# Kernel tuning notes

Measured on AMD Instinct MI355X. Metric: run time of the kernel, lower is better.

## Reference

```python
import jax, jax.numpy as jnp
import numpy as np

TOPK, ALPHA, BETA, EPS = 13, 1.0, 6.0, 1e-9
IMG = 1024.0

def _box_min_max(b):
    # b: [..., 5] cxcywhr -> per-box axis-aligned extents of rotated corners
    cx, cy, w, h, r = (b[..., i] for i in range(5))
    cos_r, sin_r = jnp.cos(r), jnp.sin(r)
    dx = w / 2 * cos_r
    dy = h / 2 * sin_r
    xc = jnp.stack([cx - dx, cx + dx, cx + dx, cx - dx], -1)
    yc = jnp.stack([cy - dy, cy - dy, cy + dy, cy + dy], -1)
    xr = cx[..., None] + (xc - cx[..., None]) * cos_r[..., None] - (yc - cy[..., None]) * sin_r[..., None]
    yr = cy[..., None] + (xc - cx[..., None]) * sin_r[..., None] + (yc - cy[..., None]) * cos_r[..., None]
    return xr.min(-1), xr.max(-1), yr.min(-1), yr.max(-1)

def batch_cxcywhr_iou(box1, box2, eps=EPS):
    # box1 [B,M1,5], box2 [B,M2,5] -> [B,M1,M2]
    mnx1, mxx1, mny1, mxy1 = (t[:, :, None] for t in _box_min_max(box1))
    mnx2, mxx2, mny2, mxy2 = (t[:, None, :] for t in _box_min_max(box2))
    iw = jnp.clip(jnp.minimum(mxx1, mxx2) - jnp.maximum(mnx1, mnx2), 0.0)
    ih = jnp.clip(jnp.minimum(mxy1, mxy2) - jnp.maximum(mny1, mny2), 0.0)
    inter = iw * ih
    a1 = (box1[..., 2] * box1[..., 3])[:, :, None]
    a2 = (box2[..., 2] * box2[..., 3])[:, None, :]
    return jnp.clip(inter / (a1 + a2 - inter + eps), 0.0, 1.0)

def check_points_inside_rboxes(points, rboxes):
    # points [L,2], rboxes [B,n,5] -> float mask [B,n,L]
    px, py = points[:, 0], points[:, 1]
    cx, cy, w, h, r = (rboxes[..., i][..., None] for i in range(5))  # [B,n,1]
    dx, dy = px - cx, py - cy
    cos_r, sin_r = jnp.cos(r), jnp.sin(r)
    xl = dx * cos_r + dy * sin_r
    yl = -dx * sin_r + dy * cos_r
    return ((jnp.abs(xl) <= w / 2) & (jnp.abs(yl) <= h / 2)).astype(jnp.float32)

def gather_topk_anchors(metrics, topk, topk_mask):
    # metrics [B,n,L] -> float {0,1} mask [B,n,L]
    B, n, L = metrics.shape
    _, idxs = jax.lax.top_k(metrics, topk)  # [B,n,topk]
    bi = jnp.arange(B)[:, None, None]
    gi = jnp.arange(n)[None, :, None]
    is_in_topk = jnp.zeros((B, n, L), metrics.dtype).at[bi, gi, idxs].add(1.0)
    return is_in_topk * topk_mask

def compute_max_iou_anchor(ious):
    # ious [B,n,L] -> one-hot over n of argmax gt per anchor, [B,n,L]
    idx = jnp.argmax(ious, axis=1)  # [B,L]
    return jnp.transpose(jax.nn.one_hot(idx, ious.shape[1], dtype=ious.dtype), (0, 2, 1))

def _make_anchor_points():
    pts = []
    for s in (8, 16, 32):
        g = int(IMG) // s
        xs = (jnp.arange(g, dtype=jnp.float32) + 0.5) * s
        yy, xx = jnp.meshgrid(xs, xs, indexing='ij')
        pts.append(jnp.stack([xx.ravel(), yy.ravel()], -1))
    return jnp.concatenate(pts, 0)  # [21504, 2]

def _rand_rboxes(key, shape, wh_lo, wh_hi):
    k1, k2, k3 = jax.random.split(key, 3)
    cxy = jax.random.uniform(k1, shape[:-1] + (2,), minval=0.0, maxval=IMG)
    wh = jax.random.uniform(k2, shape[:-1] + (2,), minval=wh_lo, maxval=wh_hi)
    r = jax.random.uniform(k3, shape[:-1] + (1,), minval=-np.pi, maxval=np.pi)
    return jnp.concatenate([cxy, wh, r], -1).astype(jnp.float32)

def setup_inputs() -> dict:
    key = jax.random.key(0)
    ks = jax.random.split(key, 6)
    B, L, C, n = 8, 21504, 15, 60
    return {
        'pred_scores': jax.random.uniform(ks[0], (B, L, C), dtype=jnp.float32),
        'pred_rboxes': _rand_rboxes(ks[1], (B, L, 5), 4.0, 120.0),
        'anchor_points': _make_anchor_points(),
        'gt_labels': jax.random.randint(ks[2], (B, n, 1), 0, C).astype(jnp.int64),
        'gt_bboxes': _rand_rboxes(ks[3], (B, n, 5), 20.0, 300.0),
        'gt_poses': jnp.zeros((B, n, 1, 3), jnp.float32),
        'gt_crowd': jax.random.randint(ks[4], (B, n, 1), 0, 2).astype(jnp.int32),
        'pad_gt_mask': jnp.ones((B, n, 1), jnp.float32),
        'bg_index': 15,
    }

def reference(pred_scores, pred_rboxes, anchor_points, gt_labels, gt_bboxes, gt_poses, gt_crowd, pad_gt_mask, bg_index):
    B, L, C = pred_scores.shape
    n = gt_bboxes.shape[1]
    labels = gt_labels[..., 0]  # [B,n]

    ious = batch_cxcywhr_iou(gt_bboxes, pred_rboxes)  # [B,n,L]
    ps = jnp.transpose(pred_scores, (0, 2, 1))  # [B,C,L]
    bbox_cls_scores = jnp.take_along_axis(ps, jnp.broadcast_to(labels[:, :, None], (B, n, L)), axis=1)
    alignment_metrics = bbox_cls_scores ** ALPHA * ious ** BETA

    is_in_gts = check_points_inside_rboxes(anchor_points, gt_bboxes)
    is_in_topk = gather_topk_anchors(alignment_metrics * is_in_gts, TOPK, pad_gt_mask)
    mask_positive = is_in_topk * is_in_gts * pad_gt_mask
    mask_positive_sum = mask_positive.sum(axis=1)  # [B,L]

    # resolve anchors assigned to multiple gts by max IoU (identity when none)
    mask_multiple = jnp.broadcast_to((mask_positive_sum[:, None, :] > 1), (B, n, L))
    mask_positive = jnp.where(mask_multiple, compute_max_iou_anchor(ious), mask_positive)
    mask_positive_sum = mask_positive.sum(axis=1)

    assigned_gt_index = jnp.argmax(mask_positive, axis=1)  # [B,L]
    flat_idx = assigned_gt_index + jnp.arange(B)[:, None] * n

    assigned_labels = labels.reshape(-1)[flat_idx]
    assigned_labels = jnp.where(mask_positive_sum > 0, assigned_labels, bg_index)

    assigned_rboxes = gt_bboxes.reshape(-1, 5)[flat_idx.reshape(-1)].reshape(B, L, 5)

    assigned_scores = jax.nn.one_hot(assigned_labels, C + 1, dtype=pred_scores.dtype)
    keep = jnp.array([i for i in range(C + 1) if i != bg_index])
    assigned_scores = assigned_scores[..., keep]

    alignment_metrics = alignment_metrics * mask_positive
    max_metrics = alignment_metrics.max(axis=-1, keepdims=True)
    max_ious = (ious * mask_positive).max(axis=-1, keepdims=True)
    alignment_metrics = alignment_metrics / (max_metrics + EPS) * max_ious
    per_anchor = alignment_metrics.max(axis=1)[..., None]  # [B,L,1]
    assigned_scores = assigned_scores * per_anchor

    assigned_crowd = gt_crowd.reshape(-1)[flat_idx.reshape(-1)].reshape(B, L)
    assigned_scores = assigned_scores * (assigned_crowd == 0)[..., None]

    return (assigned_labels, assigned_rboxes, assigned_scores, assigned_gt_index, assigned_crowd)
```

## Files before the change

### kernel.cpp

```cpp
#include <hip/hip_runtime.h>
#include <math.h>

#pragma clang fp contract(off)

#define BB   8
#define NGT  60
#define LL   21504
#define CC   15
#define KTOP 13
#define BGI  15
#define EPSF 1e-9f

typedef unsigned long long u64;

#define CS(a, b) { u64 _hi = (b > a) ? b : a; u64 _lo = (b > a) ? a : b; a = _hi; b = _lo; }

__device__ __forceinline__ float4 aabb_from_trig(float cx, float cy, float w,
                                                 float h, float cr, float sr) {
    float dx = (w * 0.5f) * cr;
    float dy = (h * 0.5f) * sr;
    float xs[4] = {cx - dx, cx + dx, cx + dx, cx - dx};
    float ys[4] = {cy - dy, cy - dy, cy + dy, cy + dy};
    float mnx = 1e30f, mxx = -1e30f, mny = 1e30f, mxy = -1e30f;
#pragma unroll
    for (int k = 0; k < 4; ++k) {
        float tx = xs[k] - cx, ty = ys[k] - cy;
        float xr = (cx + tx * cr) - ty * sr;
        float yr = (cy + tx * sr) + ty * cr;
        mnx = fminf(mnx, xr); mxx = fmaxf(mxx, xr);
        mny = fminf(mny, yr); mxy = fmaxf(mxy, yr);
    }
    return make_float4(mnx, mxx, mny, mxy);
}

__device__ __forceinline__ void trig32(float r, float& cr, float& sr) {
    double s_, c_;
    sincos((double)r, &s_, &c_);
    cr = (float)c_; sr = (float)s_;
}

__device__ __forceinline__ float4 rbox_aabb(float cx, float cy, float w, float h, float r) {
    float cr, sr; trig32(r, cr, sr);
    return aabb_from_trig(cx, cy, w, h, cr, sr);
}

__device__ __forceinline__ float iou_pair(float4 g, float a1, float4 p, float a2) {
    float iw = fmaxf(fminf(g.y, p.y) - fmaxf(g.x, p.x), 0.0f);
    float ih = fmaxf(fminf(g.w, p.w) - fmaxf(g.z, p.z), 0.0f);
    float inter = iw * ih;
    float denom = ((a1 + a2) - inter) + EPSF;
    float q = inter / denom;
    return fminf(fmaxf(q, 0.0f), 1.0f);
}

__global__ __launch_bounds__(512) void topk_kernel(
        const float* __restrict__ ps,
        const float* __restrict__ pr,
        const int*   __restrict__ labels,
        const float* __restrict__ gt,
        const float* __restrict__ pad,
        int* __restrict__ cnt,
        int* __restrict__ claim) {
    __shared__ u64   sk[8 * KTOP];
    __shared__ float sgt[12];
    __shared__ int   slab;
    const int bi = blockIdx.x;
    if (threadIdx.x == 0) {
        const float* gp = gt + (size_t)bi * 5;
        float gcx = gp[0], gcy = gp[1], gw = gp[2], gh = gp[3], gr = gp[4];
        float cr, sr; trig32(gr, cr, sr);
        float4 gb = aabb_from_trig(gcx, gcy, gw, gh, cr, sr);
        sgt[0] = gb.x; sgt[1] = gb.y; sgt[2] = gb.z; sgt[3] = gb.w;
        sgt[4] = cr;   sgt[5] = sr;
        sgt[6] = gw * gh; sgt[7] = pad[bi];
        sgt[8] = gcx; sgt[9] = gcy; sgt[10] = gw * 0.5f; sgt[11] = gh * 0.5f;
        slab = labels[bi];
    }
    __syncthreads();
    if (sgt[7] == 0.0f) return;
    const int b = bi / NGT, gi = bi % NGT;
    const float4 g  = make_float4(sgt[0], sgt[1], sgt[2], sgt[3]);
    const float4 tg = make_float4(sgt[4], sgt[5], sgt[6], 1.0f);
    const float4 gg = make_float4(sgt[8], sgt[9], sgt[10], sgt[11]);
    const float a1 = tg.z;
    const float* srow = ps + (size_t)b * LL * CC + slab;
    const float* prb  = pr + (size_t)b * LL * 5;

    const float ac  = fabsf(tg.x), asn = fabsf(tg.y);
    const float hx  = gg.z * ac + gg.w * asn + 1.0f;
    const float hy  = gg.z * asn + gg.w * ac + 1.0f;
    const float mnx = gg.x - hx, mxx = gg.x + hx;
    const float mny = gg.y - hy, mxy = gg.y + hy;

    int x0a, y0a, nxa, na;
    int x0b, y0b, nxb, nb;
    int x0c, y0c, nxc, nc;
    {
        int xa = (int)floorf(mnx * 0.125f - 0.5f);
        int xb = (int)ceilf (mxx * 0.125f - 0.5f);
        int ya = (int)floorf(mny * 0.125f - 0.5f);
        int yb = (int)ceilf (mxy * 0.125f - 0.5f);
        xa = xa > 0 ? xa : 0; xb = xb < 127 ? xb : 127;
        ya = ya > 1 ? ya : 1; yb = yb < 127 ? yb : 127;
        x0a = xa; y0a = ya;
        nxa = xb - xa + 1; if (nxa < 0) nxa = 0;
        int ny = yb - ya + 1; if (ny < 0) ny = 0;
        na = nxa * ny;
    }
    {
        int xa = (int)floorf(mnx * 0.0625f - 0.5f);
        int xb = (int)ceilf (mxx * 0.0625f - 0.5f);
        int ya = (int)floorf(mny * 0.0625f - 0.5f);
        int yb = (int)ceilf (mxy * 0.0625f - 0.5f);
        xa = xa > 0 ? xa : 0; xb = xb < 63 ? xb : 63;
        ya = ya > 0 ? ya : 0; yb = yb < 63 ? yb : 63;
        x0b = xa; y0b = ya;
        nxb = xb - xa + 1; if (nxb < 0) nxb = 0;
        int ny = yb - ya + 1; if (ny < 0) ny = 0;
        nb = nxb * ny;
    }
    {
        int xa = (int)floorf(mnx * 0.03125f - 0.5f);
        int xb = (int)ceilf (mxx * 0.03125f - 0.5f);
        int ya = (int)floorf(mny * 0.03125f - 0.5f);
        int yb = (int)ceilf (mxy * 0.03125f - 0.5f);
        xa = xa > 0 ? xa : 0; xb = xb < 31 ? xb : 31;
        ya = ya > 0 ? ya : 0; yb = yb < 31 ? yb : 31;
        x0c = xa; y0c = ya;
        nxc = xb - xa + 1; if (nxc < 0) nxc = 0;
        int ny = yb - ya + 1; if (ny < 0) ny = 0;
        nc = nxc * ny;
    }
    const int Ta = 128 + na;
    const int Tb = Ta + nb;
    const int Tc = Tb + nc;

    u64 k0 = 0, k1 = 0, k2 = 0, k3 = 0, k4 = 0, k5 = 0, k6 = 0,
        k7 = 0, k8 = 0, k9 = 0, k10 = 0, k11 = 0, k12 = 0;

    for (int e = threadIdx.x; e < Tc; e += 512) {
        int j; float ax, ay;
        if (e < 128) {
            j = e; ax = ((float)e + 0.5f) * 8.0f; ay = 4.0f;
        } else if (e < Ta) {
            int rr = e - 128;
            int q = rr / nxa, rem = rr - q * nxa;
            int iy = y0a + q, ix = x0a + rem;
            j = (iy << 7) + ix;
            ax = ((float)ix + 0.5f) * 8.0f;
            ay = ((float)iy + 0.5f) * 8.0f;
        } else if (e < Tb) {
            int rr = e - Ta;
            int q = rr / nxb, rem = rr - q * nxb;
            int iy = y0b + q, ix = x0b + rem;
            j = 16384 + (iy << 6) + ix;
            ax = ((float)ix + 0.5f) * 16.0f;
            ay = ((float)iy + 0.5f) * 16.0f;
        } else {
            int rr = e - Tb;
            int q = rr / nxc, rem = rr - q * nxc;
            int iy = y0c + q, ix = x0c + rem;
            j = 20480 + (iy << 5) + ix;
            ax = ((float)ix + 0.5f) * 32.0f;
            ay = ((float)iy + 0.5f) * 32.0f;
        }
        float dx = ax - gg.x, dy = ay - gg.y;
        float xl = dx * tg.x + dy * tg.y;
        float yl = dy * tg.x - dx * tg.y;
        bool ing = (fabsf(xl) <= gg.z) && (fabsf(yl) <= gg.w);
        float v = 0.0f;
        if (ing) {
            const float* pp = prb + (size_t)j * 5;
            float pcx = pp[0], pcy = pp[1], pw = pp[2], ph = pp[3], prr = pp[4];
            float pcr, psr; trig32(prr, pcr, psr);
            float4 p = aabb_from_trig(pcx, pcy, pw, ph, pcr, psr);
            float a2 = pw * ph;
            float iou = iou_pair(g, a1, p, a2);
            float i2 = iou * iou;
            v = srow[(size_t)j * CC] * (i2 * i2 * i2);
        }
        u64 key = ((u64)__float_as_uint(v) << 32) | (unsigned)(~j);
        if (key > k12) {
            k12 = key;
            CS(k11, k12); CS(k10, k11); CS(k9, k10); CS(k8, k9);
            CS(k7, k8);   CS(k6, k7);   CS(k5, k6);  CS(k4, k5);
            CS(k3, k4);   CS(k2, k3);   CS(k1, k2);  CS(k0, k1);
        }
    }

    const int lane = threadIdx.x & 63;
    const int wv   = threadIdx.x >> 6;
    for (int r = 0; r < KTOP; ++r) {
        u64 ov = k0;
#pragma unroll
        for (int off = 32; off > 0; off >>= 1) {
            u64 v2 = __shfl_xor(ov, off, 64);
            if (v2 > ov) ov = v2;
        }
        if (ov == 0) {
            if (lane == 0)
                for (int rr = r; rr < KTOP; ++rr) sk[wv * KTOP + rr] = 0;
            break;
        }
        if (lane == 0) sk[wv * KTOP + r] = ov;
        if (k0 == ov) {
            k0 = k1; k1 = k2; k2 = k3; k3 = k4; k4 = k5; k5 = k6; k6 = k7;
            k7 = k8; k8 = k9; k9 = k10; k10 = k11; k11 = k12; k12 = 0;
        }
    }
    __syncthreads();

    if (threadIdx.x < 64) {
        const int t = threadIdx.x;
        u64 ka = sk[t];
        u64 kb = (t < 8 * KTOP - 64) ? sk[64 + t] : 0;
        u64 mywin = 0;
        for (int r = 0; r < KTOP; ++r) {
            u64 ov = ka > kb ? ka : kb;
#pragma unroll
            for (int off = 32; off > 0; off >>= 1) {
                u64 v2 = __shfl_xor(ov, off, 64);
                if (v2 > ov) ov = v2;
            }
            if (ov == 0) break;
            if (t == r) mywin = ov;
            if (ka == ov) ka = 0;
            else if (kb == ov) kb = 0;
        }
        if (mywin != 0) {
            unsigned vb = (unsigned)(mywin >> 32);
            int j = (int)(~(unsigned)mywin);
            bool in = (vb != 0);
            if (!in) {
                int bas, gsh; float scf;
                if (j < 16384)      { bas = 0;     gsh = 7; scf = 8.0f; }
                else if (j < 20480) { bas = 16384; gsh = 6; scf = 16.0f; }
                else                { bas = 20480; gsh = 5; scf = 32.0f; }
                int rel = j - bas;
                int iy = rel >> gsh, ix = rel & ((1 << gsh) - 1);
                float ax = ((float)ix + 0.5f) * scf;
                float ay = ((float)iy + 0.5f) * scf;
                float dx = ax - gg.x, dy = ay - gg.y;
                float xl = dx * tg.x + dy * tg.y;
                float yl = dy * tg.x - dx * tg.y;
                in = (fabsf(xl) <= gg.z) && (fabsf(yl) <= gg.w);
            }
            if (in) {
                atomicAdd(&cnt[b * LL + j], 1);
                atomicMax(&claim[b * LL + j], gi);
            }
        }
    }
}

__global__ void resolve_kernel(const float* __restrict__ ps,
                               const float* __restrict__ pr,
                               const int* __restrict__ labels,
                               const float* __restrict__ gt,
                               const int* __restrict__ cnt,
                               const int* __restrict__ claim,
                               int* __restrict__ assigned,
                               float* __restrict__ aMetric,
                               unsigned* __restrict__ maxM,
                               unsigned* __restrict__ maxI) {
    __shared__ float4 sB[NGT];
    __shared__ float  sA[NGT];
    int b = blockIdx.y, t = threadIdx.x;
    if (t < NGT) {
        const float* gp = gt + (size_t)(b * NGT + t) * 5;
        float gcx = gp[0], gcy = gp[1], gw = gp[2], gh = gp[3], gr = gp[4];
        sB[t] = rbox_aabb(gcx, gcy, gw, gh, gr);
        sA[t] = gw * gh;
    }
    __syncthreads();
    int j = blockIdx.x * blockDim.x + t;
    if (j >= LL) return;
    int p = b * LL + j;
    int c = cnt[p];
    if (c == 0) { assigned[p] = -1; aMetric[p] = 0.0f; return; }
    const float* pp = pr + (size_t)p * 5;
    float pcx = pp[0], pcy = pp[1], pw = pp[2], ph = pp[3], prr = pp[4];
    float pcr, psr; trig32(prr, pcr, psr);
    float4 pb = aabb_from_trig(pcx, pcy, pw, ph, pcr, psr);
    float a2 = pw * ph;
    int a; float iouv;
    if (c == 1) {
        a = claim[p];
        iouv = iou_pair(sB[a], sA[a], pb, a2);
    } else {
        float best = -1.0f; int bi = 0;
        for (int i = 0; i < NGT; ++i) {
            float v = iou_pair(sB[i], sA[i], pb, a2);
            if (v > best) { best = v; bi = i; }
        }
        a = bi; iouv = best;
    }
    float sc = ps[(size_t)p * CC + labels[b * NGT + a]];
    float i2 = iouv * iouv;
    float m = sc * (i2 * i2 * i2);
    assigned[p] = a;
    aMetric[p] = m;
    atomicMax(&maxM[b * NGT + a], __float_as_uint(m));
    atomicMax(&maxI[b * NGT + a], __float_as_uint(iouv));
}

__global__ __launch_bounds__(256) void finalize_kernel(
        const float* __restrict__ gt,
        const int* __restrict__ labels,
        const int* __restrict__ crowd,
        const int* __restrict__ assigned,
        const float* __restrict__ aMetric,
        const unsigned* __restrict__ maxM,
        const unsigned* __restrict__ maxI,
        float* __restrict__ out) {
    __shared__ float lds[5 * 257];
    const int t = threadIdx.x;
    const int b = blockIdx.x / (LL / 256);
    const int j0 = (blockIdx.x % (LL / 256)) * 256;
    const int p = blockIdx.x * 256 + t;
    const size_t O0 = 0;
    const size_t O1 = (size_t)BB * LL;
    const size_t O2 = O1 + (size_t)BB * LL * 5;
    const size_t O3 = O2 + (size_t)BB * LL * CC;
    const size_t O4 = O3 + (size_t)BB * LL;

    int a = assigned[p];
    bool pos = (a >= 0);
    int idx = pos ? a : 0;
    int lab = labels[b * NGT + idx];
    int cw  = crowd[b * NGT + idx];
    out[O0 + p] = pos ? (float)lab : (float)BGI;
    out[O3 + p] = (float)idx;
    out[O4 + p] = (float)cw;
    if (pos && cw == 0) {
        float mm = __uint_as_float(maxM[b * NGT + a]);
        float mi = __uint_as_float(maxI[b * NGT + a]);
        float per = aMetric[p] / (mm + EPSF) * mi;
        out[O2 + (size_t)p * CC + lab] = per;
    }

    const float* gb = gt + (size_t)(b * NGT + idx) * 5;
#pragma unroll
    for (int k = 0; k < 5; ++k)
        lds[k * 257 + t] = gb[k];
    __syncthreads();
    float* o1 = out + O1 + (size_t)(b * LL + j0) * 5;
#pragma unroll
    for (int k = 0; k < 5; ++k) {
        int g = k * 256 + t;
        o1[g] = lds[(g % 5) * 257 + g / 5];
    }
}

extern "C" void kernel_launch(void* const* d_in, const int* in_sizes, int n_in,
                              void* d_out, int out_size, void* d_ws, size_t ws_size,
                              hipStream_t stream) {
    const float* pred_scores = (const float*)d_in[0];
    const float* pred_rboxes = (const float*)d_in[1];
    const int*   gt_labels   = (const int*)d_in[3];
    const float* gt_bboxes   = (const float*)d_in[4];
    const int*   gt_crowd    = (const int*)d_in[6];
    const float* pad_gt      = (const float*)d_in[7];
    float* out = (float*)d_out;

    char* ws = (char*)d_ws;
    size_t off = 0;
    auto alloc = [&](size_t bytes) {
        void* pp = ws + off;
        off += (bytes + 255) & ~(size_t)255;
        return pp;
    };
    int* cnt        = (int*)alloc((size_t)BB * LL * 4);
    int* claim      = (int*)alloc((size_t)BB * LL * 4);
    unsigned* maxM  = (unsigned*)alloc((size_t)BB * NGT * 4);
    unsigned* maxI  = (unsigned*)alloc((size_t)BB * NGT * 4);
    size_t zspan = (size_t)((char*)maxI - (char*)cnt) + (size_t)BB * NGT * 4;
    int*   assigned = (int*)alloc((size_t)BB * LL * 4);
    float* aMetric  = (float*)alloc((size_t)BB * LL * 4);

    hipMemsetAsync(cnt, 0, zspan, stream);
    topk_kernel<<<dim3(BB * NGT), dim3(512), 0, stream>>>(
        pred_scores, pred_rboxes, gt_labels, gt_bboxes, pad_gt, cnt, claim);
    resolve_kernel<<<dim3(LL / 256, BB), dim3(256), 0, stream>>>(
        pred_scores, pred_rboxes, gt_labels, gt_bboxes, cnt, claim,
        assigned, aMetric, maxM, maxI);
    finalize_kernel<<<dim3(BB * LL / 256), dim3(256), 0, stream>>>(
        gt_bboxes, gt_labels, gt_crowd, assigned, aMetric, maxM, maxI, out);
}
```

Measured before the change: 122.6 us.

## Fold default outputs into top-k kernel and resolve claims per batch in LDS

The memset, the dense per-anchor resolve kernel and the finalize kernel are replaced by two launches. Extra blocks in the top-k kernel write background defaults for every anchor. A per-batch claims kernel then dedups the top-k winners in shared memory, computes IoU, metrics and the per-GT maxima with LDS atomics, and scatters outputs only for positive anchors. This removes global atomics, workspace traffic and launch overhead. The cost is a serial claims phase of only 8 blocks, each doing an O(NW^2) duplicate scan.

```diff
diff --git a/kernel.cpp b/kernel.cpp
--- a/kernel.cpp
+++ b/kernel.cpp
@@ -10,6 +10,8 @@
 #define KTOP 13
 #define BGI  15
 #define EPSF 1e-9f
+#define NW   (NGT * KTOP)
+#define DTILE (BB * LL / 512)
 
 typedef unsigned long long u64;
 
@@ -39,11 +41,6 @@
     cr = (float)c_; sr = (float)s_;
 }
 
-__device__ __forceinline__ float4 rbox_aabb(float cx, float cy, float w, float h, float r) {
-    float cr, sr; trig32(r, cr, sr);
-    return aabb_from_trig(cx, cy, w, h, cr, sr);
-}
-
 __device__ __forceinline__ float iou_pair(float4 g, float a1, float4 p, float a2) {
     float iw = fmaxf(fminf(g.y, p.y) - fmaxf(g.x, p.x), 0.0f);
     float ih = fmaxf(fminf(g.w, p.w) - fmaxf(g.z, p.z), 0.0f);
@@ -53,19 +50,49 @@
     return fminf(fmaxf(q, 0.0f), 1.0f);
 }
 
-__global__ __launch_bounds__(512) void topk_kernel(
+#define O0 ((size_t)0)
+#define O1 ((size_t)BB * LL)
+#define O2 (O1 + (size_t)BB * LL * 5)
+#define O3 (O2 + (size_t)BB * LL * CC)
+#define O4 (O3 + (size_t)BB * LL)
+
+__global__ __launch_bounds__(512) void topk_defaults_kernel(
         const float* __restrict__ ps,
         const float* __restrict__ pr,
         const int*   __restrict__ labels,
         const float* __restrict__ gt,
+        const int*   __restrict__ crowd,
         const float* __restrict__ pad,
-        int* __restrict__ cnt,
-        int* __restrict__ claim) {
+        u64* __restrict__ win,
+        float* __restrict__ out) {
     __shared__ u64   sk[8 * KTOP];
     __shared__ float sgt[12];
     __shared__ int   slab;
-    const int bi = blockIdx.x;
-    if (threadIdx.x == 0) {
+    const int blk = blockIdx.x;
+    const int t   = threadIdx.x;
+
+    if (blk >= BB * NGT) {
+        const int dblk = blk - BB * NGT;
+        const int b  = dblk / (LL / 512);
+        const int j0 = (dblk % (LL / 512)) * 512;
+        if (t < 5)  sgt[t] = gt[(size_t)b * NGT * 5 + t];
+        if (t == 5) sgt[5] = (float)crowd[b * NGT];
+        __syncthreads();
+        const int p = b * LL + j0 + t;
+        out[O0 + p] = (float)BGI;
+        out[O3 + p] = 0.0f;
+        out[O4 + p] = sgt[5];
+        float* o1 = out + O1 + (size_t)(b * LL + j0) * 5;
+#pragma unroll
+        for (int k = 0; k < 5; ++k) {
+            int g = k * 512 + t;
+            o1[g] = sgt[g % 5];
+        }
+        return;
+    }
+
+    const int bi = blk;
+    if (t == 0) {
         const float* gp = gt + (size_t)bi * 5;
         float gcx = gp[0], gcy = gp[1], gw = gp[2], gh = gp[3], gr = gp[4];
         float cr, sr; trig32(gr, cr, sr);
@@ -77,8 +104,11 @@
         slab = labels[bi];
     }
     __syncthreads();
-    if (sgt[7] == 0.0f) return;
-    const int b = bi / NGT, gi = bi % NGT;
+    if (sgt[7] == 0.0f) {
+        if (t < KTOP) win[(size_t)bi * KTOP + t] = 0;
+        return;
+    }
+    const int b = bi / NGT;
     const float4 g  = make_float4(sgt[0], sgt[1], sgt[2], sgt[3]);
     const float4 tg = make_float4(sgt[4], sgt[5], sgt[6], 1.0f);
     const float4 gg = make_float4(sgt[8], sgt[9], sgt[10], sgt[11]);
@@ -138,7 +168,7 @@
     u64 k0 = 0, k1 = 0, k2 = 0, k3 = 0, k4 = 0, k5 = 0, k6 = 0,
         k7 = 0, k8 = 0, k9 = 0, k10 = 0, k11 = 0, k12 = 0;
 
-    for (int e = threadIdx.x; e < Tc; e += 512) {
+    for (int e = t; e < Tc; e += 512) {
         int j; float ax, ay;
         if (e < 128) {
             j = e; ax = ((float)e + 0.5f) * 8.0f; ay = 4.0f;
@@ -188,8 +218,8 @@
         }
     }
 
-    const int lane = threadIdx.x & 63;
-    const int wv   = threadIdx.x >> 6;
+    const int lane = t & 63;
+    const int wv   = t >> 6;
     for (int r = 0; r < KTOP; ++r) {
         u64 ov = k0;
 #pragma unroll
@@ -210,8 +240,7 @@
     }
     __syncthreads();
 
-    if (threadIdx.x < 64) {
-        const int t = threadIdx.x;
+    if (t < 64) {
         u64 ka = sk[t];
         u64 kb = (t < 8 * KTOP - 64) ? sk[64 + t] : 0;
         u64 mywin = 0;
@@ -227,11 +256,51 @@
             if (ka == ov) ka = 0;
             else if (kb == ov) kb = 0;
         }
-        if (mywin != 0) {
-            unsigned vb = (unsigned)(mywin >> 32);
-            int j = (int)(~(unsigned)mywin);
+        if (t < KTOP) win[(size_t)bi * KTOP + t] = mywin;
+    }
+}
+
+__global__ __launch_bounds__(512) void claims_kernel(
+        const float* __restrict__ ps,
+        const float* __restrict__ pr,
+        const int*   __restrict__ labels,
+        const float* __restrict__ gt,
+        const int*   __restrict__ crowd,
+        const u64*   __restrict__ win,
+        float* __restrict__ out) {
+    __shared__ float4 sB[NGT];
+    __shared__ float4 sG[NGT];
+    __shared__ float2 sT[NGT];
+    __shared__ float  sA[NGT];
+    __shared__ int    sL[NGT], sC[NGT];
+    __shared__ int    sj[NW];
+    __shared__ unsigned smaxM[NGT], smaxI[NGT];
+    const int b = blockIdx.x;
+    const int t = threadIdx.x;
+
+    if (t < NGT) {
+        const float* gp = gt + (size_t)(b * NGT + t) * 5;
+        float gcx = gp[0], gcy = gp[1], gw = gp[2], gh = gp[3], gr = gp[4];
+        float cr, sr; trig32(gr, cr, sr);
+        sB[t] = aabb_from_trig(gcx, gcy, gw, gh, cr, sr);
+        sG[t] = make_float4(gcx, gcy, gw * 0.5f, gh * 0.5f);
+        sT[t] = make_float2(cr, sr);
+        sA[t] = gw * gh;
+        sL[t] = labels[b * NGT + t];
+        sC[t] = crowd[b * NGT + t];
+        smaxM[t] = 0u; smaxI[t] = 0u;
+    }
+    __syncthreads();
+
+    for (int s = t; s < NW; s += 512) {
+        u64 k = win[(size_t)b * NW + s];
+        int jj = -1;
+        if (k != 0) {
+            unsigned vb = (unsigned)(k >> 32);
+            int j = (int)(~(unsigned)k);
             bool in = (vb != 0);
             if (!in) {
+                int gidx = s / KTOP;
                 int bas, gsh; float scf;
                 if (j < 16384)      { bas = 0;     gsh = 7; scf = 8.0f; }
                 else if (j < 20480) { bas = 16384; gsh = 6; scf = 16.0f; }
@@ -240,115 +309,76 @@
                 int iy = rel >> gsh, ix = rel & ((1 << gsh) - 1);
                 float ax = ((float)ix + 0.5f) * scf;
                 float ay = ((float)iy + 0.5f) * scf;
-                float dx = ax - gg.x, dy = ay - gg.y;
-                float xl = dx * tg.x + dy * tg.y;
-                float yl = dy * tg.x - dx * tg.y;
-                in = (fabsf(xl) <= gg.z) && (fabsf(yl) <= gg.w);
+                float dx = ax - sG[gidx].x, dy = ay - sG[gidx].y;
+                float xl = dx * sT[gidx].x + dy * sT[gidx].y;
+                float yl = dy * sT[gidx].x - dx * sT[gidx].y;
+                in = (fabsf(xl) <= sG[gidx].z) && (fabsf(yl) <= sG[gidx].w);
             }
-            if (in) {
-                atomicAdd(&cnt[b * LL + j], 1);
-                atomicMax(&claim[b * LL + j], gi);
+            if (in) jj = j;
+        }
+        sj[s] = jj;
+    }
+    __syncthreads();
+
+    int jA = -1, aA = 0; float mA = 0.0f;
+    int jB = -1, aB = 0; float mB = 0.0f;
+#pragma unroll
+    for (int it = 0; it < 2; ++it) {
+        int s = t + it * 512;
+        if (s >= NW) break;
+        int j = sj[s];
+        if (j < 0) continue;
+        int cntj = 0, first = NW;
+        for (int s2 = 0; s2 < NW; ++s2)
+            if (sj[s2] == j) { ++cntj; if (s2 < first) first = s2; }
+        if (first != s) continue;
+        const float* pp = pr + (size_t)(b * LL + j) * 5;
+        float pcx = pp[0], pcy = pp[1], pw = pp[2], ph = pp[3], prr = pp[4];
+        float pcr, psr; trig32(prr, pcr, psr);
+        float4 pb = aabb_from_trig(pcx, pcy, pw, ph, pcr, psr);
+        float a2 = pw * ph;
+        int a; float iouv;
+        if (cntj == 1) {
+            a = s / KTOP;
+            iouv = iou_pair(sB[a], sA[a], pb, a2);
+        } else {
+            float best = -1.0f; int bix = 0;
+            for (int i = 0; i < NGT; ++i) {
+                float v = iou_pair(sB[i], sA[i], pb, a2);
+                if (v > best) { best = v; bix = i; }
             }
-        }
-    }
-}
-
-__global__ void resolve_kernel(const float* __restrict__ ps,
-                               const float* __restrict__ pr,
-                               const int* __restrict__ labels,
-                               const float* __restrict__ gt,
-                               const int* __restrict__ cnt,
-                               const int* __restrict__ claim,
-                               int* __restrict__ assigned,
-                               float* __restrict__ aMetric,
-                               unsigned* __restrict__ maxM,
-                               unsigned* __restrict__ maxI) {
-    __shared__ float4 sB[NGT];
-    __shared__ float  sA[NGT];
-    int b = blockIdx.y, t = threadIdx.x;
-    if (t < NGT) {
-        const float* gp = gt + (size_t)(b * NGT + t) * 5;
-        float gcx = gp[0], gcy = gp[1], gw = gp[2], gh = gp[3], gr = gp[4];
-        sB[t] = rbox_aabb(gcx, gcy, gw, gh, gr);
-        sA[t] = gw * gh;
+            a = bix; iouv = best;
+        }
+        float sc = ps[(size_t)(b * LL + j) * CC + sL[a]];
+        float i2 = iouv * iouv;
+        float m = sc * (i2 * i2 * i2);
+        atomicMax(&smaxM[a], __float_as_uint(m));
+        atomicMax(&smaxI[a], __float_as_uint(iouv));
+        if (it == 0) { jA = j; aA = a; mA = m; }
+        else         { jB = j; aB = a; mB = m; }
     }
     __syncthreads();
-    int j = blockIdx.x * blockDim.x + t;
-    if (j >= LL) return;
-    int p = b * LL + j;
-    int c = cnt[p];
-    if (c == 0) { assigned[p] = -1; aMetric[p] = 0.0f; return; }
-    const float* pp = pr + (size_t)p * 5;
-    float pcx = pp[0], pcy = pp[1], pw = pp[2], ph = pp[3], prr = pp[4];
-    float pcr, psr; trig32(prr, pcr, psr);
-    float4 pb = aabb_from_trig(pcx, pcy, pw, ph, pcr, psr);
-    float a2 = pw * ph;
-    int a; float iouv;
-    if (c == 1) {
-        a = claim[p];
-        iouv = iou_pair(sB[a], sA[a], pb, a2);
-    } else {
-        float best = -1.0f; int bi = 0;
-        for (int i = 0; i < NGT; ++i) {
-            float v = iou_pair(sB[i], sA[i], pb, a2);
-            if (v > best) { best = v; bi = i; }
-        }
-        a = bi; iouv = best;
-    }
-    float sc = ps[(size_t)p * CC + labels[b * NGT + a]];
-    float i2 = iouv * iouv;
-    float m = sc * (i2 * i2 * i2);
-    assigned[p] = a;
-    aMetric[p] = m;
-    atomicMax(&maxM[b * NGT + a], __float_as_uint(m));
-    atomicMax(&maxI[b * NGT + a], __float_as_uint(iouv));
-}
-
-__global__ __launch_bounds__(256) void finalize_kernel(
-        const float* __restrict__ gt,
-        const int* __restrict__ labels,
-        const int* __restrict__ crowd,
-        const int* __restrict__ assigned,
-        const float* __restrict__ aMetric,
-        const unsigned* __restrict__ maxM,
-        const unsigned* __restrict__ maxI,
-        float* __restrict__ out) {
-    __shared__ float lds[5 * 257];
-    const int t = threadIdx.x;
-    const int b = blockIdx.x / (LL / 256);
-    const int j0 = (blockIdx.x % (LL / 256)) * 256;
-    const int p = blockIdx.x * 256 + t;
-    const size_t O0 = 0;
-    const size_t O1 = (size_t)BB * LL;
-    const size_t O2 = O1 + (size_t)BB * LL * 5;
-    const size_t O3 = O2 + (size_t)BB * LL * CC;
-    const size_t O4 = O3 + (size_t)BB * LL;
-
-    int a = assigned[p];
-    bool pos = (a >= 0);
-    int idx = pos ? a : 0;
-    int lab = labels[b * NGT + idx];
-    int cw  = crowd[b * NGT + idx];
-    out[O0 + p] = pos ? (float)lab : (float)BGI;
-    out[O3 + p] = (float)idx;
-    out[O4 + p] = (float)cw;
-    if (pos && cw == 0) {
-        float mm = __uint_as_float(maxM[b * NGT + a]);
-        float mi = __uint_as_float(maxI[b * NGT + a]);
-        float per = aMetric[p] / (mm + EPSF) * mi;
-        out[O2 + (size_t)p * CC + lab] = per;
-    }
-
-    const float* gb = gt + (size_t)(b * NGT + idx) * 5;
-#pragma unroll
-    for (int k = 0; k < 5; ++k)
-        lds[k * 257 + t] = gb[k];
-    __syncthreads();
-    float* o1 = out + O1 + (size_t)(b * LL + j0) * 5;
-#pragma unroll
-    for (int k = 0; k < 5; ++k) {
-        int g = k * 256 + t;
-        o1[g] = lds[(g % 5) * 257 + g / 5];
+
+#pragma unroll
+    for (int it = 0; it < 2; ++it) {
+        int j = (it == 0) ? jA : jB;
+        if (j < 0) continue;
+        int a   = (it == 0) ? aA : aB;
+        float m = (it == 0) ? mA : mB;
+        size_t p = (size_t)b * LL + j;
+        out[O0 + p] = (float)sL[a];
+        out[O3 + p] = (float)a;
+        out[O4 + p] = (float)sC[a];
+        const float* gb = gt + (size_t)(b * NGT + a) * 5;
+        float* o1 = out + O1 + p * 5;
+#pragma unroll
+        for (int k = 0; k < 5; ++k) o1[k] = gb[k];
+        if (sC[a] == 0) {
+            float mm = __uint_as_float(smaxM[a]);
+            float mi = __uint_as_float(smaxI[a]);
+            float per = m / (mm + EPSF) * mi;
+            out[O2 + p * CC + sL[a]] = per;
+        }
     }
 }
 
@@ -363,27 +393,11 @@
     const float* pad_gt      = (const float*)d_in[7];
     float* out = (float*)d_out;
 
-    char* ws = (char*)d_ws;
-    size_t off = 0;
-    auto alloc = [&](size_t bytes) {
-        void* pp = ws + off;
-        off += (bytes + 255) & ~(size_t)255;
-        return pp;
-    };
-    int* cnt        = (int*)alloc((size_t)BB * LL * 4);
-    int* claim      = (int*)alloc((size_t)BB * LL * 4);
-    unsigned* maxM  = (unsigned*)alloc((size_t)BB * NGT * 4);
-    unsigned* maxI  = (unsigned*)alloc((size_t)BB * NGT * 4);
-    size_t zspan = (size_t)((char*)maxI - (char*)cnt) + (size_t)BB * NGT * 4;
-    int*   assigned = (int*)alloc((size_t)BB * LL * 4);
-    float* aMetric  = (float*)alloc((size_t)BB * LL * 4);
-
-    hipMemsetAsync(cnt, 0, zspan, stream);
-    topk_kernel<<<dim3(BB * NGT), dim3(512), 0, stream>>>(
-        pred_scores, pred_rboxes, gt_labels, gt_bboxes, pad_gt, cnt, claim);
-    resolve_kernel<<<dim3(LL / 256, BB), dim3(256), 0, stream>>>(
-        pred_scores, pred_rboxes, gt_labels, gt_bboxes, cnt, claim,
-        assigned, aMetric, maxM, maxI);
-    finalize_kernel<<<dim3(BB * LL / 256), dim3(256), 0, stream>>>(
-        gt_bboxes, gt_labels, gt_crowd, assigned, aMetric, maxM, maxI, out);
-}
+    u64* win = (u64*)d_ws;
+
+    topk_defaults_kernel<<<dim3(BB * NGT + DTILE), dim3(512), 0, stream>>>(
+        pred_scores, pred_rboxes, gt_labels, gt_bboxes, gt_crowd, pad_gt,
+        win, out);
+    claims_kernel<<<dim3(BB), dim3(512), 0, stream>>>(
+        pred_scores, pred_rboxes, gt_labels, gt_bboxes, gt_crowd, win, out);
+}
```

Measured after the change: 151.9 us. +23.9%, slower.
